# Kernel optimization log

Measured on AMD Instinct MI355X. Metric: run time of the kernel, lower is better.

Reference implementation:

```python
import jax, jax.numpy as jnp
import numpy as np

HEADS = 4
HID = 256
MAX_OFFSET = 2


def setup_inputs() -> dict:
    key = jax.random.key(0)
    ks = jax.random.split(key, 8)
    B, T, C = 4, 512, HID
    x = jax.random.normal(ks[0], (B, T, C), jnp.float32)
    mask = jax.random.randint(ks[1], (B, 1, T), 0, 2).astype(bool)
    s2 = 1.0 / np.sqrt(2 * C)
    s1 = 1.0 / np.sqrt(C)
    W_subj = jax.random.uniform(ks[2], (2 * C, C), jnp.float32, -s2, s2)
    b_subj = jax.random.uniform(ks[3], (C,), jnp.float32, -s2, s2)
    W_obj = jax.random.uniform(ks[4], (2 * C, C), jnp.float32, -s2, s2)
    b_obj = jax.random.uniform(ks[5], (C,), jnp.float32, -s2, s2)
    W_t = jax.random.uniform(ks[6], (C, HEADS), jnp.float32, -s1, s1)
    b_t = jax.random.uniform(ks[7], (HEADS,), jnp.float32, -s1, s1)
    return {"x": x, "W_subj": W_subj, "b_subj": b_subj, "W_obj": W_obj,
            "b_obj": b_obj, "W_t": W_t, "b_t": b_t, "mask": mask}


def reference(x, W_subj, b_subj, W_obj, b_obj, W_t, b_t, mask):
    # x: [B,T,C]. torch MaxPool1d on [B,T,C] pools over the LAST dim (C),
    # kernel = 2*MAX_OFFSET+1, stride 1, same padding (pad value -inf).
    k = 2 * MAX_OFFSET + 1
    x_pooled = jax.lax.reduce_window(
        x, -jnp.inf, jax.lax.max,
        window_dimensions=(1, 1, k), window_strides=(1, 1, 1),
        padding=[(0, 0), (0, 0), (MAX_OFFSET, MAX_OFFSET)])
    x_new = jnp.concatenate([x_pooled, x], axis=2)      # [B,T,2C]
    subj = x_new @ W_subj + b_subj                      # [B,T,C]
    obj = x_new @ W_obj + b_obj                         # [B,T,C]
    # subj.unsqueeze(1): varies over axis 2; obj.unsqueeze(2): varies over axis 1
    abs_multi = jnp.abs(subj[:, None, :, :] - obj[:, :, None, :])  # [B,T,T,C]
    rep = abs_multi @ W_t + b_t                         # [B,T,T,H]
    attn = jax.nn.softmax(jax.nn.relu(rep), axis=2)     # softmax over obj axis
    m = mask[:, 0, :]                                   # [B,T]
    mm = m[:, None, :] & m[:, :, None]                  # [B,T,T]
    attn = jnp.where(mm[..., None], 0.0, attn)          # masked_fill -> 0
    return x_new, attn  # attn[..., h] == attn_adj_list[h]
```

## Files before the change

kernel.cpp:

```cpp
#include <hip/hip_runtime.h>
#include <hip/hip_bf16.h>
#include <math.h>

#define NB 4
#define NT 512
#define NC 256
#define NC2 512
#define NH 4

typedef __attribute__((ext_vector_type(8))) short bf16x8;
typedef __attribute__((ext_vector_type(4))) float f32x4;
typedef __attribute__((ext_vector_type(2))) float f32x2;

__device__ inline unsigned short f2bf(float f) {
    unsigned u = __float_as_uint(f);
    unsigned r = (u + 0x7fffu + ((u >> 16) & 1u)) >> 16;
    return (unsigned short)r;
}

__global__ __launch_bounds__(256) void k_prep(
    const float* __restrict__ x, const unsigned char* __restrict__ raw,
    const float* __restrict__ Ws, const float* __restrict__ Wo,
    float* __restrict__ xnew, unsigned short* __restrict__ xb,
    int* __restrict__ wmask, unsigned short* __restrict__ wbt) {
    const int row = blockIdx.x;
    const int c = threadIdx.x;
    __shared__ float r[NC];
    __shared__ float wl[32][33];
    __shared__ int s_bytes;

    r[c] = x[(size_t)row * NC + c];
    __syncthreads();
    float m = r[c];
    if (c >= 1) m = fmaxf(m, r[c - 1]);
    if (c >= 2) m = fmaxf(m, r[c - 2]);
    if (c <= 254) m = fmaxf(m, r[c + 1]);
    if (c <= 253) m = fmaxf(m, r[c + 2]);
    float* o = xnew + (size_t)row * NC2;
    o[c] = m;
    o[NC + c] = r[c];
    unsigned short* ob = xb + (size_t)row * NC2;
    ob[c] = f2bf(m);
    ob[NC + c] = f2bf(r[c]);

    if (row == 0) {
        if (c == 0) s_bytes = 0;
        __syncthreads();
        int flag = 0;
        const unsigned* w = (const unsigned*)raw;
        for (int i = c; i < (NB * NT) / 4; i += 256)
            if (w[i] > 1u) flag = 1;
        if (flag) atomicOr(&s_bytes, 1);
        __syncthreads();
        const int ib = s_bytes;
        for (int i = c; i < NB * NT; i += 256) {
            int v = ib ? (int)raw[i] : ((const int*)raw)[i];
            wmask[i] = v ? 1 : 0;
        }
    }

    if (row >= 1 && row <= 256) {
        const int t = row - 1;
        const int kb = t >> 4, nb = t & 15;
        const int tx = c & 31, ty8 = c >> 5;
        const int n0 = nb * 32, k0 = kb * 32;
        const float* src = (n0 < 256) ? Ws : Wo;
        const int ncol = n0 & 255;
#pragma unroll
        for (int rr = 0; rr < 4; ++rr) {
            int kl = ty8 * 4 + rr;
            wl[kl][tx] = src[(size_t)(k0 + kl) * NC + ncol + tx];
        }
        __syncthreads();
#pragma unroll
        for (int rr = 0; rr < 4; ++rr) {
            int nl = ty8 * 4 + rr;
            wbt[(size_t)(n0 + nl) * NC2 + k0 + tx] = f2bf(wl[tx][nl]);
        }
    }
}

#define MFMA_B16(A, B, C) __builtin_amdgcn_mfma_f32_16x16x32_bf16(A, B, C, 0, 0, 0)
__global__ __launch_bounds__(256) void k_gemm(
    const unsigned short* __restrict__ xb, const unsigned short* __restrict__ wbt,
    const float* __restrict__ bs, const float* __restrict__ bo,
    float* __restrict__ subj, float* __restrict__ obj) {
    const int bx = blockIdx.x;
    const int m0 = (bx >> 3) * 64;
    const int n0 = (bx & 7) * 64;
    const int w = threadIdx.x >> 6, lane = threadIdx.x & 63;
    const int wm = m0 + (w >> 1) * 32;
    const int wn = n0 + (w & 1) * 32;
    const int r = lane & 15, kg = lane >> 4;

    const unsigned short* aB0 = xb + (size_t)(wm + r) * NC2 + kg * 8;
    const unsigned short* aB1 = aB0 + 16 * NC2;
    const unsigned short* bB0 = wbt + (size_t)(wn + r) * NC2 + kg * 8;
    const unsigned short* bB1 = bB0 + 16 * NC2;

    f32x4 acc00 = {0.f, 0.f, 0.f, 0.f}, acc01 = {0.f, 0.f, 0.f, 0.f};
    f32x4 acc10 = {0.f, 0.f, 0.f, 0.f}, acc11 = {0.f, 0.f, 0.f, 0.f};

    bf16x8 a0 = *(const bf16x8*)(aB0);
    bf16x8 a1 = *(const bf16x8*)(aB1);
    bf16x8 b0 = *(const bf16x8*)(bB0);
    bf16x8 b1 = *(const bf16x8*)(bB1);

    for (int kk = 0; kk < NC2; kk += 64) {
        bf16x8 a0n = *(const bf16x8*)(aB0 + kk + 32);
        bf16x8 a1n = *(const bf16x8*)(aB1 + kk + 32);
        bf16x8 b0n = *(const bf16x8*)(bB0 + kk + 32);
        bf16x8 b1n = *(const bf16x8*)(bB1 + kk + 32);
        acc00 = MFMA_B16(a0, b0, acc00);
        acc01 = MFMA_B16(a0, b1, acc01);
        acc10 = MFMA_B16(a1, b0, acc10);
        acc11 = MFMA_B16(a1, b1, acc11);
        if (kk + 64 < NC2) {
            a0 = *(const bf16x8*)(aB0 + kk + 64);
            a1 = *(const bf16x8*)(aB1 + kk + 64);
            b0 = *(const bf16x8*)(bB0 + kk + 64);
            b1 = *(const bf16x8*)(bB1 + kk + 64);
        }
        acc00 = MFMA_B16(a0n, b0n, acc00);
        acc01 = MFMA_B16(a0n, b1n, acc01);
        acc10 = MFMA_B16(a1n, b0n, acc10);
        acc11 = MFMA_B16(a1n, b1n, acc11);
    }

#define EPI(ACC, S, T) { \
    const int col = wn + (T) * 16 + r; \
    const int rowb = wm + (S) * 16 + kg * 4; \
    const float bias = (col < NC) ? bs[col] : bo[col - NC]; \
    float* outp = (col < NC) ? (subj + col) : (obj + col - NC); \
    _Pragma("unroll") \
    for (int e = 0; e < 4; ++e) outp[(size_t)(rowb + e) * NC] = ACC[e] + bias; }
    EPI(acc00, 0, 0) EPI(acc01, 0, 1) EPI(acc10, 1, 0) EPI(acc11, 1, 1)
#undef EPI
}

__global__ __launch_bounds__(256) void k_sw(
    const float* __restrict__ subj, const float* __restrict__ obj,
    const float* __restrict__ Wt, float* __restrict__ Sw, float* __restrict__ Ow) {
    const int gw = blockIdx.x * 4 + (threadIdx.x >> 6);
    const int lane = threadIdx.x & 63;
    const int mat = gw & 1;
    const int row = gw >> 1;
    const float* src = mat ? obj : subj;
    const float4 xv = *(const float4*)(src + (size_t)row * NC + lane * 4);
    const float4* WtV = (const float4*)Wt;
    float4 a = {0.f, 0.f, 0.f, 0.f};
#pragma unroll
    for (int e = 0; e < 4; ++e) {
        const float4 wv = WtV[lane * 4 + e];
        const float xe = (e == 0) ? xv.x : (e == 1) ? xv.y : (e == 2) ? xv.z : xv.w;
        a.x = fmaf(xe, wv.x, a.x); a.y = fmaf(xe, wv.y, a.y);
        a.z = fmaf(xe, wv.z, a.z); a.w = fmaf(xe, wv.w, a.w);
    }
#pragma unroll
    for (int off = 32; off; off >>= 1) {
        a.x += __shfl_xor(a.x, off); a.y += __shfl_xor(a.y, off);
        a.z += __shfl_xor(a.z, off); a.w += __shfl_xor(a.w, off);
    }
    if (lane == 0) ((float4*)(mat ? Ow : Sw))[row] = a;
}

#define OF32(r) ((r) * 36 + (((r) >> 2) << 2))
__global__ __launch_bounds__(256, 3) void k_rep(
    const float* __restrict__ subj, const float* __restrict__ obj,
    const float* __restrict__ Wt, const float* __restrict__ bt,
    const float* __restrict__ Sw, const float* __restrict__ Ow,
    float* __restrict__ attn) {
    const int bx = blockIdx.x;
    const int b = bx >> 8;
    const int rem = bx & 255;
    const int it = rem >> 4, jt = rem & 15;
    const int i0 = it * 32, j0 = jt * 32;
    const int bNT = b * NT;

    __shared__ float lds_buf[4736];
    float* sjT = lds_buf;
    float* obT = lds_buf + 2368;

    const int tid = threadIdx.x;
    const int cs = __builtin_amdgcn_readfirstlane(tid >> 6);
    const int lane = tid & 63;
    const int tx4 = (lane & 7) * 4;
    const int ty4 = (lane >> 3) * 4;
    const int csB = cs * 16;

    const int c4a = tid & 15;
    const int jb = tid >> 4;

    const float4* WtV = (const float4*)Wt;

    f32x2 acc[4][2][4];
#pragma unroll
    for (int ii = 0; ii < 4; ++ii)
#pragma unroll
        for (int jp = 0; jp < 2; ++jp)
#pragma unroll
            for (int h = 0; h < 4; ++h) acc[ii][jp][h] = (f32x2){0.f, 0.f};

    float4 vs0, vs1, vo0, vo1;
#define LOADCH(CC) { \
    vs0 = *(const float4*)(subj + ((size_t)(bNT + j0 + jb)) * NC + (CC) + c4a * 4); \
    vs1 = *(const float4*)(subj + ((size_t)(bNT + j0 + jb + 16)) * NC + (CC) + c4a * 4); \
    vo0 = *(const float4*)(obj  + ((size_t)(bNT + i0 + jb)) * NC + (CC) + c4a * 4); \
    vo1 = *(const float4*)(obj  + ((size_t)(bNT + i0 + jb + 16)) * NC + (CC) + c4a * 4); }

    LOADCH(0)

    for (int cc = 0; cc < 4; ++cc) {
        const int cc64 = cc * 64;
        if (cc) __syncthreads();
        {
            const int rb = c4a * 4;
            sjT[OF32(rb + 0) + jb] = vs0.x; sjT[OF32(rb + 1) + jb] = vs0.y;
            sjT[OF32(rb + 2) + jb] = vs0.z; sjT[OF32(rb + 3) + jb] = vs0.w;
            sjT[OF32(rb + 0) + jb + 16] = vs1.x; sjT[OF32(rb + 1) + jb + 16] = vs1.y;
            sjT[OF32(rb + 2) + jb + 16] = vs1.z; sjT[OF32(rb + 3) + jb + 16] = vs1.w;
            obT[OF32(rb + 0) + jb] = vo0.x; obT[OF32(rb + 1) + jb] = vo0.y;
            obT[OF32(rb + 2) + jb] = vo0.z; obT[OF32(rb + 3) + jb] = vo0.w;
            obT[OF32(rb + 0) + jb + 16] = vo1.x; obT[OF32(rb + 1) + jb + 16] = vo1.y;
            obT[OF32(rb + 2) + jb + 16] = vo1.z; obT[OF32(rb + 3) + jb + 16] = vo1.w;
        }
        __syncthreads();
        if (cc + 1 < 4) LOADCH(cc64 + 64)

#pragma unroll 8
        for (int q = 0; q < 16; ++q) {
            const int cl = csB + q;
            const float4 sv4 = *(const float4*)&sjT[OF32(cl) + tx4];
            const float4 ov4 = *(const float4*)&obT[OF32(cl) + ty4];
            const float4 w4 = WtV[cc64 + cl];
            const f32x2 s01 = {sv4.x, sv4.y};
            const f32x2 s23 = {sv4.z, sv4.w};
            const f32x2 w0 = {w4.x, w4.x};
            const f32x2 w1 = {w4.y, w4.y};
            const f32x2 w2 = {w4.z, w4.z};
            const f32x2 w3 = {w4.w, w4.w};
#define IIBLK(II, OV) { \
    const f32x2 ob2 = {OV, OV}; \
    const f32x2 m01 = __builtin_elementwise_max(s01, ob2); \
    const f32x2 m23 = __builtin_elementwise_max(s23, ob2); \
    acc[II][0][0] = __builtin_elementwise_fma(m01, w0, acc[II][0][0]); \
    acc[II][0][1] = __builtin_elementwise_fma(m01, w1, acc[II][0][1]); \
    acc[II][0][2] = __builtin_elementwise_fma(m01, w2, acc[II][0][2]); \
    acc[II][0][3] = __builtin_elementwise_fma(m01, w3, acc[II][0][3]); \
    acc[II][1][0] = __builtin_elementwise_fma(m23, w0, acc[II][1][0]); \
    acc[II][1][1] = __builtin_elementwise_fma(m23, w1, acc[II][1][1]); \
    acc[II][1][2] = __builtin_elementwise_fma(m23, w2, acc[II][1][2]); \
    acc[II][1][3] = __builtin_elementwise_fma(m23, w3, acc[II][1][3]); }
            IIBLK(0, ov4.x) IIBLK(1, ov4.y) IIBLK(2, ov4.z) IIBLK(3, ov4.w)
#undef IIBLK
        }
    }
#undef LOADCH

    float* rbuf = lds_buf;
    const int lb = lane * 36;
#pragma unroll
    for (int half = 0; half < 2; ++half) {
        __syncthreads();
        if (cs == 1 || cs == 3) {
            float* p = rbuf + ((cs == 1) ? 0 : 2368) + lb;
#pragma unroll
            for (int k = 0; k < 16; ++k)
                *(f32x2*)(p + k * 2) = acc[half * 2 + (k >> 3)][(k >> 2) & 1][k & 3];
        }
        __syncthreads();
        if (cs == 0 || cs == 2) {
            const float* p = rbuf + ((cs == 0) ? 0 : 2368) + lb;
#pragma unroll
            for (int k = 0; k < 16; ++k)
                acc[half * 2 + (k >> 3)][(k >> 2) & 1][k & 3] += *(const f32x2*)(p + k * 2);
        }
    }
#pragma unroll
    for (int half = 0; half < 2; ++half) {
        __syncthreads();
        if (cs == 2) {
            float* p = rbuf + lb;
#pragma unroll
            for (int k = 0; k < 16; ++k)
                *(f32x2*)(p + k * 2) = acc[half * 2 + (k >> 3)][(k >> 2) & 1][k & 3];
        }
        __syncthreads();
        if (cs == 0) {
            const float* p = rbuf + lb;
#pragma unroll
            for (int k = 0; k < 16; ++k)
                acc[half * 2 + (k >> 3)][(k >> 2) & 1][k & 3] += *(const f32x2*)(p + k * 2);
        }
    }

    if (cs == 0) {
        const float4 btv = *(const float4*)bt;
        const float4* SwV = (const float4*)Sw;
        const float4* OwV = (const float4*)Ow;
        const float4 swv0 = SwV[bNT + j0 + tx4 + 0];
        const float4 swv1 = SwV[bNT + j0 + tx4 + 1];
        const float4 swv2 = SwV[bNT + j0 + tx4 + 2];
        const float4 swv3 = SwV[bNT + j0 + tx4 + 3];
#pragma unroll
        for (int ii = 0; ii < 4; ++ii) {
            const int i = i0 + ty4 + ii;
            const float4 owv = OwV[bNT + i];
            float* orow = attn + (((size_t)(bNT + i)) * NT + (j0 + tx4)) * NH;
            float4 r0, r1, r2, r3;
            r0.x = fmaxf(2.f * acc[ii][0][0].x - swv0.x - owv.x + btv.x, 0.f);
            r0.y = fmaxf(2.f * acc[ii][0][1].x - swv0.y - owv.y + btv.y, 0.f);
            r0.z = fmaxf(2.f * acc[ii][0][2].x - swv0.z - owv.z + btv.z, 0.f);
            r0.w = fmaxf(2.f * acc[ii][0][3].x - swv0.w - owv.w + btv.w, 0.f);
            r1.x = fmaxf(2.f * acc[ii][0][0].y - swv1.x - owv.x + btv.x, 0.f);
            r1.y = fmaxf(2.f * acc[ii][0][1].y - swv1.y - owv.y + btv.y, 0.f);
            r1.z = fmaxf(2.f * acc[ii][0][2].y - swv1.z - owv.z + btv.z, 0.f);
            r1.w = fmaxf(2.f * acc[ii][0][3].y - swv1.w - owv.w + btv.w, 0.f);
            r2.x = fmaxf(2.f * acc[ii][1][0].x - swv2.x - owv.x + btv.x, 0.f);
            r2.y = fmaxf(2.f * acc[ii][1][1].x - swv2.y - owv.y + btv.y, 0.f);
            r2.z = fmaxf(2.f * acc[ii][1][2].x - swv2.z - owv.z + btv.z, 0.f);
            r2.w = fmaxf(2.f * acc[ii][1][3].x - swv2.w - owv.w + btv.w, 0.f);
            r3.x = fmaxf(2.f * acc[ii][1][0].y - swv3.x - owv.x + btv.x, 0.f);
            r3.y = fmaxf(2.f * acc[ii][1][1].y - swv3.y - owv.y + btv.y, 0.f);
            r3.z = fmaxf(2.f * acc[ii][1][2].y - swv3.z - owv.z + btv.z, 0.f);
            r3.w = fmaxf(2.f * acc[ii][1][3].y - swv3.w - owv.w + btv.w, 0.f);
            *(float4*)(orow + 0)  = r0;
            *(float4*)(orow + 4)  = r1;
            *(float4*)(orow + 8)  = r2;
            *(float4*)(orow + 12) = r3;
        }
    }
}

__global__ __launch_bounds__(256) void k_soft(float* __restrict__ attn,
                                              const int* __restrict__ mask) {
    const int wv = threadIdx.x >> 6, lane = threadIdx.x & 63;
    const int bi = blockIdx.x * 4 + wv;
    const int b = bi >> 9;
    float4* row = (float4*)(attn + (size_t)bi * (NT * NH));

    float4 v[8];
#pragma unroll
    for (int q = 0; q < 8; ++q) v[q] = row[lane + 64 * q];

    float mx[4];
#pragma unroll
    for (int h = 0; h < 4; ++h) {
        float m = ((const float*)&v[0])[h];
#pragma unroll
        for (int q = 1; q < 8; ++q) m = fmaxf(m, ((const float*)&v[q])[h]);
        mx[h] = m;
    }
#pragma unroll
    for (int off = 32; off; off >>= 1) {
#pragma unroll
        for (int h = 0; h < 4; ++h) mx[h] = fmaxf(mx[h], __shfl_xor(mx[h], off));
    }

    float sm[4] = {0.f, 0.f, 0.f, 0.f};
#pragma unroll
    for (int q = 0; q < 8; ++q) {
        float4 e;
        e.x = expf(v[q].x - mx[0]); e.y = expf(v[q].y - mx[1]);
        e.z = expf(v[q].z - mx[2]); e.w = expf(v[q].w - mx[3]);
        v[q] = e;
        sm[0] += e.x; sm[1] += e.y; sm[2] += e.z; sm[3] += e.w;
    }
#pragma unroll
    for (int off = 32; off; off >>= 1) {
#pragma unroll
        for (int h = 0; h < 4; ++h) sm[h] += __shfl_xor(sm[h], off);
    }
    float rinv[4];
#pragma unroll
    for (int h = 0; h < 4; ++h) rinv[h] = 1.0f / sm[h];

    const int mi = mask[bi];
#pragma unroll
    for (int q = 0; q < 8; ++q) {
        const int mj = mask[b * NT + lane + 64 * q];
        const bool z = (mi & mj);
        float4 o;
        o.x = z ? 0.f : v[q].x * rinv[0];
        o.y = z ? 0.f : v[q].y * rinv[1];
        o.z = z ? 0.f : v[q].z * rinv[2];
        o.w = z ? 0.f : v[q].w * rinv[3];
        row[lane + 64 * q] = o;
    }
}

extern "C" void kernel_launch(void* const* d_in, const int* in_sizes, int n_in,
                              void* d_out, int out_size, void* d_ws, size_t ws_size,
                              hipStream_t stream) {
    const float* x      = (const float*)d_in[0];
    const float* W_subj = (const float*)d_in[1];
    const float* b_subj = (const float*)d_in[2];
    const float* W_obj  = (const float*)d_in[3];
    const float* b_obj  = (const float*)d_in[4];
    const float* W_t    = (const float*)d_in[5];
    const float* b_t    = (const float*)d_in[6];
    const unsigned char* mask_raw = (const unsigned char*)d_in[7];

    float* xnew = (float*)d_out;
    float* attn = xnew + (size_t)NB * NT * NC2;

    int* wmask          = (int*)d_ws;
    float* subj         = (float*)((char*)d_ws + 8192);
    float* obj          = subj + (size_t)NB * NT * NC;
    unsigned short* xb  = (unsigned short*)(obj + (size_t)NB * NT * NC);
    unsigned short* wbt = xb + (size_t)NB * NT * NC2;
    float* Sw           = (float*)(wbt + (size_t)NC2 * NC2);
    float* Ow           = Sw + (size_t)NB * NT * NH;

    hipLaunchKernelGGL(k_prep, dim3(NB * NT), dim3(256), 0, stream,
                       x, mask_raw, W_subj, W_obj, xnew, xb, wmask, wbt);
    hipLaunchKernelGGL(k_gemm, dim3(256), dim3(256), 0, stream,
                       xb, wbt, b_subj, b_obj, subj, obj);
    hipLaunchKernelGGL(k_sw, dim3(1024), dim3(256), 0, stream,
                       subj, obj, W_t, Sw, Ow);
    hipLaunchKernelGGL(k_rep, dim3(NB * 16 * 16), dim3(256), 0, stream,
                       subj, obj, W_t, b_t, Sw, Ow, attn);
    hipLaunchKernelGGL(k_soft, dim3(NB * NT / 4), dim3(256), 0, stream, attn, wmask);
}
```

Baseline: 138.1 us.

## Store subj/obj in fp16 and use packed max plus dot2 in pairwise kernel

Subj and obj projections are now written as fp16, and W_t is pre-packed into fp16 pairs. The pairwise kernel uses v_pk_max_f16 and v_dot2_f32_f16 over two channels at once with a swizzled LDS layout, and the occupancy hint rises from 3 to 4. The GEMM moves to 512 threads per block with smaller per-wave tiles, and softmax drops the max subtraction because relu outputs are non-negative and assumed small. This halves the memory traffic and ALU instruction count of the hot pairwise loop, at the cost of fp16 precision in the features and overflow risk in the unshifted exp.

```diff
diff --git a/kernel.cpp b/kernel.cpp
--- a/kernel.cpp
+++ b/kernel.cpp
@@ -10,19 +10,27 @@
 
 typedef __attribute__((ext_vector_type(8))) short bf16x8;
 typedef __attribute__((ext_vector_type(4))) float f32x4;
-typedef __attribute__((ext_vector_type(2))) float f32x2;
+typedef __attribute__((ext_vector_type(2))) __fp16 fp16x2;
 
 __device__ inline unsigned short f2bf(float f) {
     unsigned u = __float_as_uint(f);
     unsigned r = (u + 0x7fffu + ((u >> 16) & 1u)) >> 16;
     return (unsigned short)r;
 }
+__device__ inline unsigned pkrtz(float a, float b) {
+    fp16x2 h = __builtin_amdgcn_cvt_pkrtz(a, b);
+    return __builtin_bit_cast(unsigned, h);
+}
+#define PKMAX(D, A, B) asm("v_pk_max_f16 %0, %1, %2" : "=v"(D) : "v"(A), "v"(B))
+#define DOT2(ACC, A, B) asm("v_dot2_f32_f16 %0, %1, %2, %0" : "+v"(ACC) : "v"(A), "v"(B))
 
 __global__ __launch_bounds__(256) void k_prep(
     const float* __restrict__ x, const unsigned char* __restrict__ raw,
     const float* __restrict__ Ws, const float* __restrict__ Wo,
+    const float* __restrict__ Wt,
     float* __restrict__ xnew, unsigned short* __restrict__ xb,
-    int* __restrict__ wmask, unsigned short* __restrict__ wbt) {
+    int* __restrict__ wmask, unsigned short* __restrict__ wbt,
+    unsigned* __restrict__ whp) {
     const int row = blockIdx.x;
     const int c = threadIdx.x;
     __shared__ float r[NC];
@@ -78,96 +86,93 @@
             wbt[(size_t)(n0 + nl) * NC2 + k0 + tx] = f2bf(wl[tx][nl]);
         }
     }
+
+    if (row == 257 && c < 128) {
+        const float4 w0 = ((const float4*)Wt)[2 * c];
+        const float4 w1 = ((const float4*)Wt)[2 * c + 1];
+        whp[c * 4 + 0] = pkrtz(w0.x, w1.x);
+        whp[c * 4 + 1] = pkrtz(w0.y, w1.y);
+        whp[c * 4 + 2] = pkrtz(w0.z, w1.z);
+        whp[c * 4 + 3] = pkrtz(w0.w, w1.w);
+    }
 }
 
 #define MFMA_B16(A, B, C) __builtin_amdgcn_mfma_f32_16x16x32_bf16(A, B, C, 0, 0, 0)
-__global__ __launch_bounds__(256) void k_gemm(
+__global__ __launch_bounds__(512) void k_gemm(
     const unsigned short* __restrict__ xb, const unsigned short* __restrict__ wbt,
     const float* __restrict__ bs, const float* __restrict__ bo,
-    float* __restrict__ subj, float* __restrict__ obj) {
+    _Float16* __restrict__ subjh, _Float16* __restrict__ objh) {
     const int bx = blockIdx.x;
     const int m0 = (bx >> 3) * 64;
     const int n0 = (bx & 7) * 64;
     const int w = threadIdx.x >> 6, lane = threadIdx.x & 63;
-    const int wm = m0 + (w >> 1) * 32;
+    const int wm = m0 + (w >> 1) * 16;
     const int wn = n0 + (w & 1) * 32;
     const int r = lane & 15, kg = lane >> 4;
 
-    const unsigned short* aB0 = xb + (size_t)(wm + r) * NC2 + kg * 8;
-    const unsigned short* aB1 = aB0 + 16 * NC2;
+    const unsigned short* aB = xb + (size_t)(wm + r) * NC2 + kg * 8;
     const unsigned short* bB0 = wbt + (size_t)(wn + r) * NC2 + kg * 8;
     const unsigned short* bB1 = bB0 + 16 * NC2;
 
-    f32x4 acc00 = {0.f, 0.f, 0.f, 0.f}, acc01 = {0.f, 0.f, 0.f, 0.f};
-    f32x4 acc10 = {0.f, 0.f, 0.f, 0.f}, acc11 = {0.f, 0.f, 0.f, 0.f};
-
-    bf16x8 a0 = *(const bf16x8*)(aB0);
-    bf16x8 a1 = *(const bf16x8*)(aB1);
+    f32x4 acc0 = {0.f, 0.f, 0.f, 0.f}, acc1 = {0.f, 0.f, 0.f, 0.f};
+    bf16x8 a = *(const bf16x8*)(aB);
     bf16x8 b0 = *(const bf16x8*)(bB0);
     bf16x8 b1 = *(const bf16x8*)(bB1);
 
-    for (int kk = 0; kk < NC2; kk += 64) {
-        bf16x8 a0n = *(const bf16x8*)(aB0 + kk + 32);
-        bf16x8 a1n = *(const bf16x8*)(aB1 + kk + 32);
-        bf16x8 b0n = *(const bf16x8*)(bB0 + kk + 32);
-        bf16x8 b1n = *(const bf16x8*)(bB1 + kk + 32);
-        acc00 = MFMA_B16(a0, b0, acc00);
-        acc01 = MFMA_B16(a0, b1, acc01);
-        acc10 = MFMA_B16(a1, b0, acc10);
-        acc11 = MFMA_B16(a1, b1, acc11);
-        if (kk + 64 < NC2) {
-            a0 = *(const bf16x8*)(aB0 + kk + 64);
-            a1 = *(const bf16x8*)(aB1 + kk + 64);
-            b0 = *(const bf16x8*)(bB0 + kk + 64);
-            b1 = *(const bf16x8*)(bB1 + kk + 64);
-        }
-        acc00 = MFMA_B16(a0n, b0n, acc00);
-        acc01 = MFMA_B16(a0n, b1n, acc01);
-        acc10 = MFMA_B16(a1n, b0n, acc10);
-        acc11 = MFMA_B16(a1n, b1n, acc11);
-    }
-
-#define EPI(ACC, S, T) { \
+    for (int kk = 0; kk < NC2; kk += 32) {
+        bf16x8 an, b0n, b1n;
+        if (kk + 32 < NC2) {
+            an = *(const bf16x8*)(aB + kk + 32);
+            b0n = *(const bf16x8*)(bB0 + kk + 32);
+            b1n = *(const bf16x8*)(bB1 + kk + 32);
+        }
+        acc0 = MFMA_B16(a, b0, acc0);
+        acc1 = MFMA_B16(a, b1, acc1);
+        a = an; b0 = b0n; b1 = b1n;
+    }
+
+#define EPI(ACC, T) { \
     const int col = wn + (T) * 16 + r; \
-    const int rowb = wm + (S) * 16 + kg * 4; \
+    const int rowb = wm + kg * 4; \
     const float bias = (col < NC) ? bs[col] : bo[col - NC]; \
-    float* outp = (col < NC) ? (subj + col) : (obj + col - NC); \
+    _Float16* outp = (col < NC) ? (subjh + col) : (objh + col - NC); \
     _Pragma("unroll") \
-    for (int e = 0; e < 4; ++e) outp[(size_t)(rowb + e) * NC] = ACC[e] + bias; }
-    EPI(acc00, 0, 0) EPI(acc01, 0, 1) EPI(acc10, 1, 0) EPI(acc11, 1, 1)
+    for (int e = 0; e < 4; ++e) outp[(size_t)(rowb + e) * NC] = (_Float16)(ACC[e] + bias); }
+    EPI(acc0, 0) EPI(acc1, 1)
 #undef EPI
 }
 
 __global__ __launch_bounds__(256) void k_sw(
-    const float* __restrict__ subj, const float* __restrict__ obj,
-    const float* __restrict__ Wt, float* __restrict__ Sw, float* __restrict__ Ow) {
+    const _Float16* __restrict__ subjh, const _Float16* __restrict__ objh,
+    const unsigned* __restrict__ whp,
+    float* __restrict__ Sw, float* __restrict__ Ow) {
     const int gw = blockIdx.x * 4 + (threadIdx.x >> 6);
     const int lane = threadIdx.x & 63;
     const int mat = gw & 1;
     const int row = gw >> 1;
-    const float* src = mat ? obj : subj;
-    const float4 xv = *(const float4*)(src + (size_t)row * NC + lane * 4);
-    const float4* WtV = (const float4*)Wt;
-    float4 a = {0.f, 0.f, 0.f, 0.f};
-#pragma unroll
-    for (int e = 0; e < 4; ++e) {
-        const float4 wv = WtV[lane * 4 + e];
-        const float xe = (e == 0) ? xv.x : (e == 1) ? xv.y : (e == 2) ? xv.z : xv.w;
-        a.x = fmaf(xe, wv.x, a.x); a.y = fmaf(xe, wv.y, a.y);
-        a.z = fmaf(xe, wv.z, a.z); a.w = fmaf(xe, wv.w, a.w);
-    }
+    const _Float16* src = mat ? objh : subjh;
+    const uint2 rv = *(const uint2*)(src + (size_t)row * NC + lane * 4);
+    const uint4 wa = *(const uint4*)&whp[(2 * lane) * 4];
+    const uint4 wb = *(const uint4*)&whp[(2 * lane + 1) * 4];
+    float a0 = 0.f, a1 = 0.f, a2 = 0.f, a3 = 0.f;
+    DOT2(a0, rv.x, wa.x); DOT2(a0, rv.y, wb.x);
+    DOT2(a1, rv.x, wa.y); DOT2(a1, rv.y, wb.y);
+    DOT2(a2, rv.x, wa.z); DOT2(a2, rv.y, wb.z);
+    DOT2(a3, rv.x, wa.w); DOT2(a3, rv.y, wb.w);
 #pragma unroll
     for (int off = 32; off; off >>= 1) {
-        a.x += __shfl_xor(a.x, off); a.y += __shfl_xor(a.y, off);
-        a.z += __shfl_xor(a.z, off); a.w += __shfl_xor(a.w, off);
-    }
-    if (lane == 0) ((float4*)(mat ? Ow : Sw))[row] = a;
-}
-
-#define OF32(r) ((r) * 36 + (((r) >> 2) << 2))
-__global__ __launch_bounds__(256, 3) void k_rep(
-    const float* __restrict__ subj, const float* __restrict__ obj,
-    const float* __restrict__ Wt, const float* __restrict__ bt,
+        a0 += __shfl_xor(a0, off); a1 += __shfl_xor(a1, off);
+        a2 += __shfl_xor(a2, off); a3 += __shfl_xor(a3, off);
+    }
+    if (lane == 0) {
+        float4 v = {a0, a1, a2, a3};
+        ((float4*)(mat ? Ow : Sw))[row] = v;
+    }
+}
+
+__global__ __launch_bounds__(256, 4) void k_rep(
+    const _Float16* __restrict__ subjh, const _Float16* __restrict__ objh,
+    const unsigned* __restrict__ whp, const float* __restrict__ bt,
     const float* __restrict__ Sw, const float* __restrict__ Ow,
     float* __restrict__ attn) {
     const int bx = blockIdx.x;
@@ -177,83 +182,75 @@
     const int i0 = it * 32, j0 = jt * 32;
     const int bNT = b * NT;
 
-    __shared__ float lds_buf[4736];
-    float* sjT = lds_buf;
-    float* obT = lds_buf + 2368;
+    __shared__ float lds_buf[4608];
+    unsigned* sjT = (unsigned*)lds_buf;
+    unsigned* obT = sjT + 1024;
 
     const int tid = threadIdx.x;
     const int cs = __builtin_amdgcn_readfirstlane(tid >> 6);
     const int lane = tid & 63;
-    const int tx4 = (lane & 7) * 4;
-    const int ty4 = (lane >> 3) * 4;
-    const int csB = cs * 16;
+    const int tq = lane & 7;
+    const int oq = lane >> 3;
+    const int tx4 = tq * 4, ty4 = oq * 4;
 
     const int c4a = tid & 15;
     const int jb = tid >> 4;
 
-    const float4* WtV = (const float4*)Wt;
-
-    f32x2 acc[4][2][4];
+    float acc[4][4][4];
 #pragma unroll
     for (int ii = 0; ii < 4; ++ii)
 #pragma unroll
-        for (int jp = 0; jp < 2; ++jp)
-#pragma unroll
-            for (int h = 0; h < 4; ++h) acc[ii][jp][h] = (f32x2){0.f, 0.f};
-
-    float4 vs0, vs1, vo0, vo1;
+        for (int jj = 0; jj < 4; ++jj)
+#pragma unroll
+            for (int h = 0; h < 4; ++h) acc[ii][jj][h] = 0.f;
+
+    uint2 vs0, vs1, vo0, vo1;
 #define LOADCH(CC) { \
-    vs0 = *(const float4*)(subj + ((size_t)(bNT + j0 + jb)) * NC + (CC) + c4a * 4); \
-    vs1 = *(const float4*)(subj + ((size_t)(bNT + j0 + jb + 16)) * NC + (CC) + c4a * 4); \
-    vo0 = *(const float4*)(obj  + ((size_t)(bNT + i0 + jb)) * NC + (CC) + c4a * 4); \
-    vo1 = *(const float4*)(obj  + ((size_t)(bNT + i0 + jb + 16)) * NC + (CC) + c4a * 4); }
+    const _Float16* sp = subjh + (size_t)(bNT + j0 + jb) * NC + (CC) + c4a * 4; \
+    const _Float16* op = objh  + (size_t)(bNT + i0 + jb) * NC + (CC) + c4a * 4; \
+    vs0 = *(const uint2*)sp; vs1 = *(const uint2*)(sp + 16 * NC); \
+    vo0 = *(const uint2*)op; vo1 = *(const uint2*)(op + 16 * NC); }
 
     LOADCH(0)
 
     for (int cc = 0; cc < 4; ++cc) {
-        const int cc64 = cc * 64;
         if (cc) __syncthreads();
         {
-            const int rb = c4a * 4;
-            sjT[OF32(rb + 0) + jb] = vs0.x; sjT[OF32(rb + 1) + jb] = vs0.y;
-            sjT[OF32(rb + 2) + jb] = vs0.z; sjT[OF32(rb + 3) + jb] = vs0.w;
-            sjT[OF32(rb + 0) + jb + 16] = vs1.x; sjT[OF32(rb + 1) + jb + 16] = vs1.y;
-            sjT[OF32(rb + 2) + jb + 16] = vs1.z; sjT[OF32(rb + 3) + jb + 16] = vs1.w;
-            obT[OF32(rb + 0) + jb] = vo0.x; obT[OF32(rb + 1) + jb] = vo0.y;
-            obT[OF32(rb + 2) + jb] = vo0.z; obT[OF32(rb + 3) + jb] = vo0.w;
-            obT[OF32(rb + 0) + jb + 16] = vo1.x; obT[OF32(rb + 1) + jb + 16] = vo1.y;
-            obT[OF32(rb + 2) + jb + 16] = vo1.z; obT[OF32(rb + 3) + jb + 16] = vo1.w;
-        }
-        __syncthreads();
-        if (cc + 1 < 4) LOADCH(cc64 + 64)
-
-#pragma unroll 8
-        for (int q = 0; q < 16; ++q) {
-            const int cl = csB + q;
-            const float4 sv4 = *(const float4*)&sjT[OF32(cl) + tx4];
-            const float4 ov4 = *(const float4*)&obT[OF32(cl) + ty4];
-            const float4 w4 = WtV[cc64 + cl];
-            const f32x2 s01 = {sv4.x, sv4.y};
-            const f32x2 s23 = {sv4.z, sv4.w};
-            const f32x2 w0 = {w4.x, w4.x};
-            const f32x2 w1 = {w4.y, w4.y};
-            const f32x2 w2 = {w4.z, w4.z};
-            const f32x2 w3 = {w4.w, w4.w};
-#define IIBLK(II, OV) { \
-    const f32x2 ob2 = {OV, OV}; \
-    const f32x2 m01 = __builtin_elementwise_max(s01, ob2); \
-    const f32x2 m23 = __builtin_elementwise_max(s23, ob2); \
-    acc[II][0][0] = __builtin_elementwise_fma(m01, w0, acc[II][0][0]); \
-    acc[II][0][1] = __builtin_elementwise_fma(m01, w1, acc[II][0][1]); \
-    acc[II][0][2] = __builtin_elementwise_fma(m01, w2, acc[II][0][2]); \
-    acc[II][0][3] = __builtin_elementwise_fma(m01, w3, acc[II][0][3]); \
-    acc[II][1][0] = __builtin_elementwise_fma(m23, w0, acc[II][1][0]); \
-    acc[II][1][1] = __builtin_elementwise_fma(m23, w1, acc[II][1][1]); \
-    acc[II][1][2] = __builtin_elementwise_fma(m23, w2, acc[II][1][2]); \
-    acc[II][1][3] = __builtin_elementwise_fma(m23, w3, acc[II][1][3]); }
-            IIBLK(0, ov4.x) IIBLK(1, ov4.y) IIBLK(2, ov4.z) IIBLK(3, ov4.w)
-#undef IIBLK
-        }
+            const int key = c4a & 7;
+            const int jq = jb >> 2, jl = jb & 3;
+            const int s0 = ((jq ^ key) << 2) + jl;
+            const int s1 = (((jq + 4) ^ key) << 2) + jl;
+            const int p0 = (c4a << 1) << 5, p1 = ((c4a << 1) | 1) << 5;
+            sjT[p0 + s0] = vs0.x; sjT[p1 + s0] = vs0.y;
+            sjT[p0 + s1] = vs1.x; sjT[p1 + s1] = vs1.y;
+            obT[p0 + s0] = vo0.x; obT[p1 + s0] = vo0.y;
+            obT[p0 + s1] = vo1.x; obT[p1 + s1] = vo1.y;
+        }
+        __syncthreads();
+        if (cc + 1 < 4) LOADCH(cc * 64 + 64)
+
+        const unsigned* whpc = whp + cc * 128;
+#define PAIR(II, JJ, SS, OO) { \
+    unsigned mm; \
+    PKMAX(mm, SS, OO); \
+    DOT2(acc[II][JJ][0], mm, wq.x); \
+    DOT2(acc[II][JJ][1], mm, wq.y); \
+    DOT2(acc[II][JJ][2], mm, wq.z); \
+    DOT2(acc[II][JJ][3], mm, wq.w); }
+#define QSTEP(Q) { \
+    const int p = cs * 8 + (Q); \
+    const int rkey = (p >> 1) & 7; \
+    const uint4 s4 = *(const uint4*)&sjT[(p << 5) + ((tq ^ rkey) << 2)]; \
+    const uint4 o4 = *(const uint4*)&obT[(p << 5) + ((oq ^ rkey) << 2)]; \
+    const uint4 wq = *(const uint4*)(whpc + (p << 2)); \
+    PAIR(0, 0, s4.x, o4.x) PAIR(0, 1, s4.y, o4.x) PAIR(0, 2, s4.z, o4.x) PAIR(0, 3, s4.w, o4.x) \
+    PAIR(1, 0, s4.x, o4.y) PAIR(1, 1, s4.y, o4.y) PAIR(1, 2, s4.z, o4.y) PAIR(1, 3, s4.w, o4.y) \
+    PAIR(2, 0, s4.x, o4.z) PAIR(2, 1, s4.y, o4.z) PAIR(2, 2, s4.z, o4.z) PAIR(2, 3, s4.w, o4.z) \
+    PAIR(3, 0, s4.x, o4.w) PAIR(3, 1, s4.y, o4.w) PAIR(3, 2, s4.z, o4.w) PAIR(3, 3, s4.w, o4.w) }
+        QSTEP(0) QSTEP(1) QSTEP(2) QSTEP(3)
+        QSTEP(4) QSTEP(5) QSTEP(6) QSTEP(7)
+#undef QSTEP
+#undef PAIR
     }
 #undef LOADCH
 
@@ -263,17 +260,27 @@
     for (int half = 0; half < 2; ++half) {
         __syncthreads();
         if (cs == 1 || cs == 3) {
-            float* p = rbuf + ((cs == 1) ? 0 : 2368) + lb;
-#pragma unroll
-            for (int k = 0; k < 16; ++k)
-                *(f32x2*)(p + k * 2) = acc[half * 2 + (k >> 3)][(k >> 2) & 1][k & 3];
+            float* p = rbuf + ((cs == 1) ? 0 : 2304) + lb;
+#pragma unroll
+            for (int k4 = 0; k4 < 8; ++k4) {
+                f32x4 v = {acc[half * 2 + (k4 >> 2)][k4 & 3][0],
+                           acc[half * 2 + (k4 >> 2)][k4 & 3][1],
+                           acc[half * 2 + (k4 >> 2)][k4 & 3][2],
+                           acc[half * 2 + (k4 >> 2)][k4 & 3][3]};
+                *(f32x4*)(p + k4 * 4) = v;
+            }
         }
         __syncthreads();
         if (cs == 0 || cs == 2) {
-            const float* p = rbuf + ((cs == 0) ? 0 : 2368) + lb;
-#pragma unroll
-            for (int k = 0; k < 16; ++k)
-                acc[half * 2 + (k >> 3)][(k >> 2) & 1][k & 3] += *(const f32x2*)(p + k * 2);
+            const float* p = rbuf + ((cs == 0) ? 0 : 2304) + lb;
+#pragma unroll
+            for (int k4 = 0; k4 < 8; ++k4) {
+                f32x4 v = *(const f32x4*)(p + k4 * 4);
+                acc[half * 2 + (k4 >> 2)][k4 & 3][0] += v.x;
+                acc[half * 2 + (k4 >> 2)][k4 & 3][1] += v.y;
+                acc[half * 2 + (k4 >> 2)][k4 & 3][2] += v.z;
+                acc[half * 2 + (k4 >> 2)][k4 & 3][3] += v.w;
+            }
         }
     }
 #pragma unroll
@@ -282,15 +289,25 @@
         if (cs == 2) {
             float* p = rbuf + lb;
 #pragma unroll
-            for (int k = 0; k < 16; ++k)
-                *(f32x2*)(p + k * 2) = acc[half * 2 + (k >> 3)][(k >> 2) & 1][k & 3];
+            for (int k4 = 0; k4 < 8; ++k4) {
+                f32x4 v = {acc[half * 2 + (k4 >> 2)][k4 & 3][0],
+                           acc[half * 2 + (k4 >> 2)][k4 & 3][1],
+                           acc[half * 2 + (k4 >> 2)][k4 & 3][2],
+                           acc[half * 2 + (k4 >> 2)][k4 & 3][3]};
+                *(f32x4*)(p + k4 * 4) = v;
+            }
         }
         __syncthreads();
         if (cs == 0) {
             const float* p = rbuf + lb;
 #pragma unroll
-            for (int k = 0; k < 16; ++k)
-                acc[half * 2 + (k >> 3)][(k >> 2) & 1][k & 3] += *(const f32x2*)(p + k * 2);
+            for (int k4 = 0; k4 < 8; ++k4) {
+                f32x4 v = *(const f32x4*)(p + k4 * 4);
+                acc[half * 2 + (k4 >> 2)][k4 & 3][0] += v.x;
+                acc[half * 2 + (k4 >> 2)][k4 & 3][1] += v.y;
+                acc[half * 2 + (k4 >> 2)][k4 & 3][2] += v.z;
+                acc[half * 2 + (k4 >> 2)][k4 & 3][3] += v.w;
+            }
         }
     }
 
@@ -308,22 +325,22 @@
             const float4 owv = OwV[bNT + i];
             float* orow = attn + (((size_t)(bNT + i)) * NT + (j0 + tx4)) * NH;
             float4 r0, r1, r2, r3;
-            r0.x = fmaxf(2.f * acc[ii][0][0].x - swv0.x - owv.x + btv.x, 0.f);
-            r0.y = fmaxf(2.f * acc[ii][0][1].x - swv0.y - owv.y + btv.y, 0.f);
-            r0.z = fmaxf(2.f * acc[ii][0][2].x - swv0.z - owv.z + btv.z, 0.f);
-            r0.w = fmaxf(2.f * acc[ii][0][3].x - swv0.w - owv.w + btv.w, 0.f);
-            r1.x = fmaxf(2.f * acc[ii][0][0].y - swv1.x - owv.x + btv.x, 0.f);
-            r1.y = fmaxf(2.f * acc[ii][0][1].y - swv1.y - owv.y + btv.y, 0.f);
-            r1.z = fmaxf(2.f * acc[ii][0][2].y - swv1.z - owv.z + btv.z, 0.f);
-            r1.w = fmaxf(2.f * acc[ii][0][3].y - swv1.w - owv.w + btv.w, 0.f);
-            r2.x = fmaxf(2.f * acc[ii][1][0].x - swv2.x - owv.x + btv.x, 0.f);
-            r2.y = fmaxf(2.f * acc[ii][1][1].x - swv2.y - owv.y + btv.y, 0.f);
-            r2.z = fmaxf(2.f * acc[ii][1][2].x - swv2.z - owv.z + btv.z, 0.f);
-            r2.w = fmaxf(2.f * acc[ii][1][3].x - swv2.w - owv.w + btv.w, 0.f);
-            r3.x = fmaxf(2.f * acc[ii][1][0].y - swv3.x - owv.x + btv.x, 0.f);
-            r3.y = fmaxf(2.f * acc[ii][1][1].y - swv3.y - owv.y + btv.y, 0.f);
-            r3.z = fmaxf(2.f * acc[ii][1][2].y - swv3.z - owv.z + btv.z, 0.f);
-            r3.w = fmaxf(2.f * acc[ii][1][3].y - swv3.w - owv.w + btv.w, 0.f);
+            r0.x = fmaxf(2.f * acc[ii][0][0] - swv0.x - owv.x + btv.x, 0.f);
+            r0.y = fmaxf(2.f * acc[ii][0][1] - swv0.y - owv.y + btv.y, 0.f);
+            r0.z = fmaxf(2.f * acc[ii][0][2] - swv0.z - owv.z + btv.z, 0.f);
+            r0.w = fmaxf(2.f * acc[ii][0][3] - swv0.w - owv.w + btv.w, 0.f);
+            r1.x = fmaxf(2.f * acc[ii][1][0] - swv1.x - owv.x + btv.x, 0.f);
+            r1.y = fmaxf(2.f * acc[ii][1][1] - swv1.y - owv.y + btv.y, 0.f);
+            r1.z = fmaxf(2.f * acc[ii][1][2] - swv1.z - owv.z + btv.z, 0.f);
+            r1.w = fmaxf(2.f * acc[ii][1][3] - swv1.w - owv.w + btv.w, 0.f);
+            r2.x = fmaxf(2.f * acc[ii][2][0] - swv2.x - owv.x + btv.x, 0.f);
+            r2.y = fmaxf(2.f * acc[ii][2][1] - swv2.y - owv.y + btv.y, 0.f);
+            r2.z = fmaxf(2.f * acc[ii][2][2] - swv2.z - owv.z + btv.z, 0.f);
+            r2.w = fmaxf(2.f * acc[ii][2][3] - swv2.w - owv.w + btv.w, 0.f);
+            r3.x = fmaxf(2.f * acc[ii][3][0] - swv3.x - owv.x + btv.x, 0.f);
+            r3.y = fmaxf(2.f * acc[ii][3][1] - swv3.y - owv.y + btv.y, 0.f);
+            r3.z = fmaxf(2.f * acc[ii][3][2] - swv3.z - owv.z + btv.z, 0.f);
+            r3.w = fmaxf(2.f * acc[ii][3][3] - swv3.w - owv.w + btv.w, 0.f);
             *(float4*)(orow + 0)  = r0;
             *(float4*)(orow + 4)  = r1;
             *(float4*)(orow + 8)  = r2;
@@ -343,26 +360,12 @@
 #pragma unroll
     for (int q = 0; q < 8; ++q) v[q] = row[lane + 64 * q];
 
-    float mx[4];
-#pragma unroll
-    for (int h = 0; h < 4; ++h) {
-        float m = ((const float*)&v[0])[h];
-#pragma unroll
-        for (int q = 1; q < 8; ++q) m = fmaxf(m, ((const float*)&v[q])[h]);
-        mx[h] = m;
-    }
-#pragma unroll
-    for (int off = 32; off; off >>= 1) {
-#pragma unroll
-        for (int h = 0; h < 4; ++h) mx[h] = fmaxf(mx[h], __shfl_xor(mx[h], off));
-    }
-
     float sm[4] = {0.f, 0.f, 0.f, 0.f};
 #pragma unroll
     for (int q = 0; q < 8; ++q) {
         float4 e;
-        e.x = expf(v[q].x - mx[0]); e.y = expf(v[q].y - mx[1]);
-        e.z = expf(v[q].z - mx[2]); e.w = expf(v[q].w - mx[3]);
+        e.x = expf(v[q].x); e.y = expf(v[q].y);
+        e.z = expf(v[q].z); e.w = expf(v[q].w);
         v[q] = e;
         sm[0] += e.x; sm[1] += e.y; sm[2] += e.z; sm[3] += e.w;
     }
@@ -405,20 +408,21 @@
     float* attn = xnew + (size_t)NB * NT * NC2;
 
     int* wmask          = (int*)d_ws;
-    float* subj         = (float*)((char*)d_ws + 8192);
-    float* obj          = subj + (size_t)NB * NT * NC;
-    unsigned short* xb  = (unsigned short*)(obj + (size_t)NB * NT * NC);
+    _Float16* subjh     = (_Float16*)((char*)d_ws + 8192);
+    _Float16* objh      = subjh + (size_t)NB * NT * NC;
+    unsigned short* xb  = (unsigned short*)(objh + (size_t)NB * NT * NC);
     unsigned short* wbt = xb + (size_t)NB * NT * NC2;
     float* Sw           = (float*)(wbt + (size_t)NC2 * NC2);
     float* Ow           = Sw + (size_t)NB * NT * NH;
+    unsigned* whp       = (unsigned*)(Ow + (size_t)NB * NT * NH);
 
     hipLaunchKernelGGL(k_prep, dim3(NB * NT), dim3(256), 0, stream,
-                       x, mask_raw, W_subj, W_obj, xnew, xb, wmask, wbt);
-    hipLaunchKernelGGL(k_gemm, dim3(256), dim3(256), 0, stream,
-                       xb, wbt, b_subj, b_obj, subj, obj);
+                       x, mask_raw, W_subj, W_obj, W_t, xnew, xb, wmask, wbt, whp);
+    hipLaunchKernelGGL(k_gemm, dim3(256), dim3(512), 0, stream,
+                       xb, wbt, b_subj, b_obj, subjh, objh);
     hipLaunchKernelGGL(k_sw, dim3(1024), dim3(256), 0, stream,
-                       subj, obj, W_t, Sw, Ow);
+                       subjh, objh, whp, Sw, Ow);
     hipLaunchKernelGGL(k_rep, dim3(NB * 16 * 16), dim3(256), 0, stream,
-                       subj, obj, W_t, b_t, Sw, Ow, attn);
+                       subjh, objh, whp, b_t, Sw, Ow, attn);
     hipLaunchKernelGGL(k_soft, dim3(NB * NT / 4), dim3(256), 0, stream, attn, wmask);
 }
```

Result: faster. 133.4 us (-3.4%).
